# Kernel tuning notes

Measured on AMD Instinct MI355X. Metric: run time of the kernel, lower is better.

Reference implementation:

```python
import jax, jax.numpy as jnp
import numpy as np

ALPHA = 0.25
GAMMA = 2.0
B, A, C, M = 8, 120000, 80, 32


def setup_inputs() -> dict:
    key = jax.random.key(0)
    k1, k2, k3, k4, k5, k6 = jax.random.split(key, 6)
    classifications = jax.random.uniform(k1, (B, A, C), jnp.float32)
    regressions = jax.random.normal(k2, (B, A, 4), jnp.float32)
    # anchors: valid x1<x2, y1<y2 boxes in a 1024x1024 image
    cx = jax.random.uniform(k3, (A,), jnp.float32, 0.0, 1024.0)
    cy = jax.random.uniform(k4, (A,), jnp.float32, 0.0, 1024.0)
    w = jax.random.uniform(jax.random.fold_in(k3, 1), (A,), jnp.float32, 16.0, 256.0)
    h = jax.random.uniform(jax.random.fold_in(k4, 1), (A,), jnp.float32, 16.0, 256.0)
    anchors = jnp.stack([cx - 0.5 * w, cy - 0.5 * h, cx + 0.5 * w, cy + 0.5 * h], axis=1)[None]
    # annotations: [x1,y1,x2,y2,label], all valid (label in [0, C))
    gcx = jax.random.uniform(k5, (B, M), jnp.float32, 64.0, 960.0)
    gcy = jax.random.uniform(jax.random.fold_in(k5, 1), (B, M), jnp.float32, 64.0, 960.0)
    gw = jax.random.uniform(jax.random.fold_in(k5, 2), (B, M), jnp.float32, 16.0, 256.0)
    gh = jax.random.uniform(jax.random.fold_in(k5, 3), (B, M), jnp.float32, 16.0, 256.0)
    labels = jax.random.randint(k6, (B, M), 0, C).astype(jnp.float32)
    annotations = jnp.stack(
        [gcx - 0.5 * gw, gcy - 0.5 * gh, gcx + 0.5 * gw, gcy + 0.5 * gh, labels], axis=2)
    return dict(classifications=classifications, regressions=regressions,
                anchors=anchors, annotations=annotations)


def _calc_iou(a, b):
    # a: [A,4] anchors, b: [M,4] gt boxes -> [A,M]
    area = (b[:, 2] - b[:, 0]) * (b[:, 3] - b[:, 1])
    iw = jnp.minimum(a[:, 2, None], b[None, :, 2]) - jnp.maximum(a[:, 0, None], b[None, :, 0])
    ih = jnp.minimum(a[:, 3, None], b[None, :, 3]) - jnp.maximum(a[:, 1, None], b[None, :, 1])
    inter = jnp.clip(iw, 0.0) * jnp.clip(ih, 0.0)
    ua = ((a[:, 2] - a[:, 0]) * (a[:, 3] - a[:, 1]))[:, None] + area[None, :] - inter
    return inter / jnp.clip(ua, 1e-8)


def _per_image(cls, reg, annots, anchor):
    valid = annots[:, 4] != -1.0  # padded gt boxes (label == -1) are ignored
    num_valid = valid.sum()
    cls = jnp.clip(cls, 1e-4, 1.0 - 1e-4)
    iou = jnp.where(valid[None, :], _calc_iou(anchor, annots[:, :4]), -1.0)  # [A,M]
    iou_max = iou.max(axis=1)
    iou_argmax = iou.argmax(axis=1)
    positive = iou_max >= 0.5
    num_pos = positive.sum()
    assigned = annots[iou_argmax]  # [A,5]
    nclass = cls.shape[1]
    # targets: -1 ignore; 0 where IoU<0.4 or positive; one-hot 1 at gt class for positives
    targets = jnp.full(cls.shape, -1.0, cls.dtype)
    targets = jnp.where((iou_max < 0.4)[:, None], 0.0, targets)
    onehot = jax.nn.one_hot(assigned[:, 4].astype(jnp.int32), nclass, dtype=cls.dtype)
    targets = jnp.where(positive[:, None], onehot, targets)
    alpha_factor = jnp.where(targets == 1.0, ALPHA, 1.0 - ALPHA)
    focal_w = alpha_factor * jnp.where(targets == 1.0, 1.0 - cls, cls) ** GAMMA
    bce = -(targets * jnp.log(cls) + (1.0 - targets) * jnp.log(1.0 - cls))
    cls_loss_mat = jnp.where(targets != -1.0, focal_w * bce, 0.0)
    npos_f = num_pos.astype(cls.dtype)
    cls_loss = cls_loss_mat.sum() / jnp.maximum(npos_f, 1.0)
    aw = anchor[:, 2] - anchor[:, 0]
    ah = anchor[:, 3] - anchor[:, 1]
    acx = anchor[:, 0] + 0.5 * aw
    acy = anchor[:, 1] + 0.5 * ah
    gw = assigned[:, 2] - assigned[:, 0]
    gh = assigned[:, 3] - assigned[:, 1]
    gcx = assigned[:, 0] + 0.5 * gw
    gcy = assigned[:, 1] + 0.5 * gh
    gw = jnp.maximum(gw, 1.0)
    gh = jnp.maximum(gh, 1.0)
    t = jnp.stack([(gcx - acx) / aw, (gcy - acy) / ah,
                   jnp.log(gw / aw), jnp.log(gh / ah)], axis=1)
    t = t / jnp.array([[0.1, 0.1, 0.2, 0.2]], t.dtype)
    diff = jnp.abs(t - reg)
    rl = jnp.where(diff <= 1.0 / 9.0, 0.5 * 9.0 * diff * diff, diff - 0.5 / 9.0)
    rl = jnp.where(positive[:, None], rl, 0.0)
    reg_loss = rl.sum() / jnp.maximum(npos_f * 4.0, 1.0)  # mean over [num_pos,4]
    reg_loss = jnp.where(num_pos > 0, reg_loss, 0.0)
    has = num_valid > 0
    return jnp.where(has, cls_loss, 0.0), jnp.where(has, reg_loss, 0.0)


def reference(classifications, regressions, anchors, annotations):
    anchor = anchors[0]
    cls_l, reg_l = jax.vmap(lambda c, r, a: _per_image(c, r, a, anchor))(
        classifications, regressions, annotations)
    return cls_l.mean(keepdims=True), reg_l.mean(keepdims=True)
```

## Files before the change

kernel.cpp:

```cpp
#include <hip/hip_runtime.h>

constexpr int B_IMG = 8;
constexpr int A_N   = 120000;
constexpr int C_N   = 80;
constexpr int M_N   = 32;

constexpr float ALPHA = 0.25f;

constexpr int BLK    = 256;
constexpr int APB    = 512;
constexpr int NBLK   = (A_N + APB - 1) / APB;
constexpr int F4PA   = C_N / 4;
constexpr int UNROLL = 8;
constexpr int FAST_ITERS = (APB * F4PA) / (BLK * UNROLL);

__device__ __forceinline__ float smooth_l1(float d) {
    d = fabsf(d);
    return (d <= (1.0f / 9.0f)) ? 4.5f * d * d : d - (0.5f / 9.0f);
}

__device__ __forceinline__ float loss_neg(float x) {
    float p = fminf(fmaxf(x, 1e-4f), 0.9999f);
    return (1.0f - ALPHA) * p * p * (-__logf(1.0f - p));
}

__device__ __forceinline__ float loss_pos(float x) {
    float p = fminf(fmaxf(x, 1e-4f), 0.9999f);
    float q = 1.0f - p;
    return ALPHA * q * q * (-__logf(p));
}

__device__ __forceinline__ signed char assign_one(
    const float4 anc, const float* __restrict__ ann,
    const float4* __restrict__ regs, int b, int a,
    float& regl, int& pcount)
{
    const float ax1 = anc.x, ay1 = anc.y, ax2 = anc.z, ay2 = anc.w;
    const float areaA = (ax2 - ax1) * (ay2 - ay1);

    float bi = -1.0f;
    float bu = 1.0f;
    int   bm = -1;
    #pragma unroll 2
    for (int m = 0; m < M_N; ++m) {
        const float gx1 = ann[m * 5 + 0];
        const float gy1 = ann[m * 5 + 1];
        const float gx2 = ann[m * 5 + 2];
        const float gy2 = ann[m * 5 + 3];
        const bool valid = (ann[m * 5 + 4] != -1.0f);
        float iw = fminf(ax2, gx2) - fmaxf(ax1, gx1);
        float ih = fminf(ay2, gy2) - fmaxf(ay1, gy1);
        iw = fmaxf(iw, 0.0f);
        ih = fmaxf(ih, 0.0f);
        const float inter = iw * ih;
        const float areaB = (gx2 - gx1) * (gy2 - gy1);
        const float ua = fmaxf(areaA + areaB - inter, 1e-8f);
        const bool better = valid && (inter * bu > bi * ua);
        if (better) { bi = inter; bu = ua; bm = m; }
    }

    const float iouMax = (bm >= 0) ? (bi / bu) : -1.0f;
    const bool positive = (iouMax >= 0.5f);

    if (positive) {
        pcount += 1;
        const float aw  = ax2 - ax1;
        const float ah  = ay2 - ay1;
        const float acx = ax1 + 0.5f * aw;
        const float acy = ay1 + 0.5f * ah;
        const float gx1 = ann[bm * 5 + 0];
        const float gy1 = ann[bm * 5 + 1];
        const float gx2 = ann[bm * 5 + 2];
        const float gy2 = ann[bm * 5 + 3];
        float gw = gx2 - gx1;
        float gh = gy2 - gy1;
        const float gcx = gx1 + 0.5f * gw;
        const float gcy = gy1 + 0.5f * gh;
        gw = fmaxf(gw, 1.0f);
        gh = fmaxf(gh, 1.0f);
        const float t0 = ((gcx - acx) / aw) * 10.0f;
        const float t1 = ((gcy - acy) / ah) * 10.0f;
        const float t2 = __logf(gw / aw) * 5.0f;
        const float t3 = __logf(gh / ah) * 5.0f;
        const float4 rg = regs[(size_t)b * A_N + a];
        regl += smooth_l1(t0 - rg.x) + smooth_l1(t1 - rg.y) +
                smooth_l1(t2 - rg.z) + smooth_l1(t3 - rg.w);
    }

    if (iouMax < 0.4f) return -1;
    if (positive)      return (signed char)(int)ann[bm * 5 + 4];
    return -2;
}

__global__ __launch_bounds__(BLK, 4) void fused_kernel(
    const float* __restrict__ cls,
    const float* __restrict__ regressions,
    const float* __restrict__ anchors,
    const float* __restrict__ annotations,
    float* __restrict__ clsPart,
    float* __restrict__ regPart,
    float* __restrict__ nposPart)
{
    const int b    = blockIdx.y;
    const int base = blockIdx.x * APB;
    const int nA   = min(APB, A_N - base);
    const float* __restrict__ ann = annotations + (size_t)b * M_N * 5;
    const float4* __restrict__ regs = (const float4*)regressions;

    __shared__ signed char scode[APB];
    __shared__ float       smask[APB];

    float regl = 0.0f;
    int   pcnt = 0;
    const int t = threadIdx.x;
    #pragma unroll 1
    for (int s = 0; s < APB; s += BLK) {
        const int li = s + t;
        const int a  = base + li;
        signed char c = -2;
        if (li < nA) {
            const float4 anc = ((const float4*)anchors)[a];
            c = assign_one(anc, ann, regs, b, a, regl, pcnt);
        }
        scode[li] = c;
        smask[li] = (c != -2) ? 1.0f : 0.0f;
    }
    __syncthreads();

    const float* __restrict__ rowbase = cls + (size_t)(b * A_N + base) * C_N;
    float csum = 0.0f;

    #pragma unroll 1
    for (int s = 0; s < APB; s += BLK) {
        const int li = s + t;
        const int code = scode[li];
        if (code >= 0) {
            const float x = rowbase[(size_t)li * C_N + code];
            csum += loss_pos(x) - loss_neg(x);
        }
    }

    const float4* __restrict__ src = (const float4*)rowbase;
    if (nA == APB) {
        const float4* p = src + t;
        #pragma unroll 1
        for (int it = 0; it < FAST_ITERS; ++it) {
            float4 v[UNROLL];
            #pragma unroll
            for (int u = 0; u < UNROLL; ++u) v[u] = p[u * BLK];
            const int ibase = it * (BLK * UNROLL) + t;
            #pragma unroll
            for (int u = 0; u < UNROLL; ++u) {
                const unsigned idx = (unsigned)(ibase + u * BLK);
                const float m = smask[idx / 20u];
                csum += m * (loss_neg(v[u].x) + loss_neg(v[u].y) +
                             loss_neg(v[u].z) + loss_neg(v[u].w));
            }
            p += BLK * UNROLL;
        }
    } else {
        const int nF4 = nA * F4PA;
        for (int idx = t; idx < nF4; idx += BLK) {
            const float4 v = src[idx];
            const float m = smask[(unsigned)idx / 20u];
            csum += m * (loss_neg(v.x) + loss_neg(v.y) +
                         loss_neg(v.z) + loss_neg(v.w));
        }
    }

    float r = regl, p = (float)pcnt, c = csum;
    #pragma unroll
    for (int off = 32; off; off >>= 1) {
        r += __shfl_down(r, off);
        p += __shfl_down(p, off);
        c += __shfl_down(c, off);
    }
    __shared__ float wr[BLK / 64], wp[BLK / 64], wc[BLK / 64];
    const int wid = t >> 6;
    if ((t & 63) == 0) { wr[wid] = r; wp[wid] = p; wc[wid] = c; }
    __syncthreads();
    if (t == 0) {
        float rr = 0.0f, pp = 0.0f, cc = 0.0f;
        #pragma unroll
        for (int w = 0; w < BLK / 64; ++w) { rr += wr[w]; pp += wp[w]; cc += wc[w]; }
        const int pidx = b * NBLK + blockIdx.x;
        clsPart[pidx]  = cc;
        regPart[pidx]  = rr;
        nposPart[pidx] = pp;
    }
}

__global__ __launch_bounds__(64 * B_IMG) void finalize_kernel(
    const float* __restrict__ annotations,
    const float* __restrict__ clsPart,
    const float* __restrict__ regPart,
    const float* __restrict__ nposPart,
    float* __restrict__ out)
{
    const int w    = threadIdx.x >> 6;
    const int lane = threadIdx.x & 63;

    float c = 0.0f, r = 0.0f, p = 0.0f;
    for (int i = lane; i < NBLK; i += 64) {
        const int idx = w * NBLK + i;
        c += clsPart[idx];
        r += regPart[idx];
        p += nposPart[idx];
    }
    #pragma unroll
    for (int off = 32; off; off >>= 1) {
        c += __shfl_down(c, off);
        r += __shfl_down(r, off);
        p += __shfl_down(p, off);
    }

    __shared__ float sc[B_IMG], sr[B_IMG];
    if (lane == 0) {
        bool has = false;
        for (int m = 0; m < M_N; ++m)
            has = has || (annotations[(size_t)w * M_N * 5 + m * 5 + 4] != -1.0f);
        const float cl = c / fmaxf(p, 1.0f);
        const float rl = (p > 0.0f) ? r / (p * 4.0f) : 0.0f;
        sc[w] = has ? cl : 0.0f;
        sr[w] = has ? rl : 0.0f;
    }
    __syncthreads();
    if (threadIdx.x == 0) {
        float ca = 0.0f, ra = 0.0f;
        #pragma unroll
        for (int i = 0; i < B_IMG; ++i) { ca += sc[i]; ra += sr[i]; }
        out[0] = ca * (1.0f / B_IMG);
        out[1] = ra * (1.0f / B_IMG);
    }
}

extern "C" void kernel_launch(void* const* d_in, const int* in_sizes, int n_in,
                              void* d_out, int out_size, void* d_ws, size_t ws_size,
                              hipStream_t stream) {
    const float* classifications = (const float*)d_in[0];
    const float* regressions     = (const float*)d_in[1];
    const float* anchors         = (const float*)d_in[2];
    const float* annotations     = (const float*)d_in[3];
    float* out = (float*)d_out;

    float* clsPart  = (float*)d_ws;
    float* regPart  = clsPart + (size_t)B_IMG * NBLK;
    float* nposPart = regPart + (size_t)B_IMG * NBLK;

    fused_kernel<<<dim3(NBLK, B_IMG), BLK, 0, stream>>>(
        classifications, regressions, anchors, annotations,
        clsPart, regPart, nposPart);

    finalize_kernel<<<1, 64 * B_IMG, 0, stream>>>(
        annotations, clsPart, regPart, nposPart, out);
}
```

Measured before the change: 78.07 us.

## Prefetch classification tiles during IoU assignment and double-buffer streaming loop

The first chunk of classification data is now loaded before the anchor-to-GT assignment phase, so memory latency overlaps with the IoU compute. The streaming loop becomes a two-stage ping-pong (vA/vB) with a smaller unroll, and it uses nontemporal loads so the single-use data does not pollute the cache. Each wave now covers a contiguous per-wave region rather than a block-strided one. The cost is more live registers across the assignment phase, which may lower occupancy under the launch bound of 4.

New measurement: 74.22 us. 1.05x faster.

```diff
diff --git a/kernel.cpp b/kernel.cpp
--- a/kernel.cpp
+++ b/kernel.cpp
@@ -7,12 +7,19 @@
 
 constexpr float ALPHA = 0.25f;
 
-constexpr int BLK    = 256;
-constexpr int APB    = 512;
-constexpr int NBLK   = (A_N + APB - 1) / APB;
-constexpr int F4PA   = C_N / 4;
-constexpr int UNROLL = 8;
-constexpr int FAST_ITERS = (APB * F4PA) / (BLK * UNROLL);
+constexpr int BLK  = 256;
+constexpr int APB  = 512;
+constexpr int NBLK = (A_N + APB - 1) / APB;
+constexpr int F4PA = C_N / 4;
+constexpr int U    = 4;
+constexpr int F4_PER_IT = BLK * U;
+constexpr int NIT  = (APB * F4PA) / F4_PER_IT;
+
+typedef float f4v __attribute__((ext_vector_type(4)));
+
+__device__ __forceinline__ f4v ntload(const f4v* p) {
+    return __builtin_nontemporal_load(p);
+}
 
 __device__ __forceinline__ float smooth_l1(float d) {
     d = fabsf(d);
@@ -22,6 +29,10 @@
 __device__ __forceinline__ float loss_neg(float x) {
     float p = fminf(fmaxf(x, 1e-4f), 0.9999f);
     return (1.0f - ALPHA) * p * p * (-__logf(1.0f - p));
+}
+
+__device__ __forceinline__ float loss_neg4(f4v v) {
+    return loss_neg(v[0]) + loss_neg(v[1]) + loss_neg(v[2]) + loss_neg(v[3]);
 }
 
 __device__ __forceinline__ float loss_pos(float x) {
@@ -110,9 +121,24 @@
     __shared__ signed char scode[APB];
     __shared__ float       smask[APB];
 
+    const int t    = threadIdx.x;
+    const int wave = t >> 6;
+    const int lane = t & 63;
+    const bool full = (nA == APB);
+
+    const float* __restrict__ rowbase = cls + (size_t)(b * A_N + base) * C_N;
+    const f4v* __restrict__ src = (const f4v*)rowbase;
+    const f4v* __restrict__ pw = src + wave * (64 * U) + lane;
+    const int widx0 = wave * (64 * U) + lane;
+
+    f4v vA[U], vB[U];
+    if (full) {
+        #pragma unroll
+        for (int u = 0; u < U; ++u) vA[u] = ntload(pw + u * 64);
+    }
+
     float regl = 0.0f;
     int   pcnt = 0;
-    const int t = threadIdx.x;
     #pragma unroll 1
     for (int s = 0; s < APB; s += BLK) {
         const int li = s + t;
@@ -127,7 +153,6 @@
     }
     __syncthreads();
 
-    const float* __restrict__ rowbase = cls + (size_t)(b * A_N + base) * C_N;
     float csum = 0.0f;
 
     #pragma unroll 1
@@ -140,31 +165,34 @@
         }
     }
 
-    const float4* __restrict__ src = (const float4*)rowbase;
-    if (nA == APB) {
-        const float4* p = src + t;
+    if (full) {
         #pragma unroll 1
-        for (int it = 0; it < FAST_ITERS; ++it) {
-            float4 v[UNROLL];
+        for (int it2 = 0; it2 < NIT / 2; ++it2) {
+            const int it = it2 * 2;
             #pragma unroll
-            for (int u = 0; u < UNROLL; ++u) v[u] = p[u * BLK];
-            const int ibase = it * (BLK * UNROLL) + t;
+            for (int u = 0; u < U; ++u)
+                vB[u] = ntload(pw + (it + 1) * F4_PER_IT + u * 64);
             #pragma unroll
-            for (int u = 0; u < UNROLL; ++u) {
-                const unsigned idx = (unsigned)(ibase + u * BLK);
-                const float m = smask[idx / 20u];
-                csum += m * (loss_neg(v[u].x) + loss_neg(v[u].y) +
-                             loss_neg(v[u].z) + loss_neg(v[u].w));
+            for (int u = 0; u < U; ++u) {
+                const unsigned idx = (unsigned)(it * F4_PER_IT + widx0 + u * 64);
+                csum += smask[idx / 20u] * loss_neg4(vA[u]);
             }
-            p += BLK * UNROLL;
+            if (it + 2 < NIT) {
+                #pragma unroll
+                for (int u = 0; u < U; ++u)
+                    vA[u] = ntload(pw + (it + 2) * F4_PER_IT + u * 64);
+            }
+            #pragma unroll
+            for (int u = 0; u < U; ++u) {
+                const unsigned idx = (unsigned)((it + 1) * F4_PER_IT + widx0 + u * 64);
+                csum += smask[idx / 20u] * loss_neg4(vB[u]);
+            }
         }
     } else {
         const int nF4 = nA * F4PA;
         for (int idx = t; idx < nF4; idx += BLK) {
-            const float4 v = src[idx];
-            const float m = smask[(unsigned)idx / 20u];
-            csum += m * (loss_neg(v.x) + loss_neg(v.y) +
-                         loss_neg(v.z) + loss_neg(v.w));
+            const f4v v = src[idx];
+            csum += smask[(unsigned)idx / 20u] * loss_neg4(v);
         }
     }
 
@@ -176,8 +204,7 @@
         c += __shfl_down(c, off);
     }
     __shared__ float wr[BLK / 64], wp[BLK / 64], wc[BLK / 64];
-    const int wid = t >> 6;
-    if ((t & 63) == 0) { wr[wid] = r; wp[wid] = p; wc[wid] = c; }
+    if (lane == 0) { wr[wave] = r; wp[wave] = p; wc[wave] = c; }
     __syncthreads();
     if (t == 0) {
         float rr = 0.0f, pp = 0.0f, cc = 0.0f;
```
